# Performance work log

Hardware: AMD Instinct MI355X
Metric: run time of the kernel (lower is better)

Reference implementation:

```python
import jax, jax.numpy as jnp
import numpy as np


def gcn_conv(x, src, dst, W, b, n_nodes):
    """PyG GCNConv: out = D^-1/2 (A+I) D^-1/2 (x @ W) + b.
    src/dst already include self loops. Shapes: x [N,F], src/dst [E+N].
    """
    h = x @ W  # [N, H] - linear transform first (PyG order)
    # symmetric normalization from (unweighted) degree of A + I
    deg = jax.ops.segment_sum(jnp.ones_like(dst, dtype=h.dtype), dst,
                              num_segments=n_nodes)  # [N]
    dis = jnp.where(deg > 0, jax.lax.rsqrt(deg), 0.0)  # deg_inv_sqrt, inf->0
    norm = dis[src] * dis[dst]  # [E+N]
    msg = h[src] * norm[:, None]  # gather + scale  [E+N, H]
    out = jax.ops.segment_sum(msg, dst, num_segments=n_nodes)  # scatter-add
    return out + b


def setup_inputs() -> dict:
    key = jax.random.key(0)
    ks = jax.random.split(key, 4)
    N, E, F, H, C = 50000, 1600000, 768, 128, 2
    x = jax.random.normal(ks[0], (N, F), dtype=jnp.float32)
    edge_index = jax.random.randint(ks[1], (2, E), 0, N, dtype=jnp.int64)
    W1 = jax.random.normal(ks[2], (F, H), dtype=jnp.float32) * (1.0 / np.sqrt(F))
    b1 = jnp.zeros((H,), dtype=jnp.float32)
    W2 = jax.random.normal(ks[3], (H, C), dtype=jnp.float32) * (1.0 / np.sqrt(H))
    b2 = jnp.zeros((C,), dtype=jnp.float32)
    return {"x": x, "edge_index": edge_index, "W1": W1, "b1": b1,
            "W2": W2, "b2": b2}


def reference(x, edge_index, W1, b1, W2, b2):
    n_nodes = x.shape[0]
    # add self loops once (PyG GCNConv default add_self_loops=True)
    loops = jnp.arange(n_nodes, dtype=edge_index.dtype)
    src = jnp.concatenate([edge_index[0], loops])
    dst = jnp.concatenate([edge_index[1], loops])
    h = jax.nn.relu(gcn_conv(x, src, dst, W1, b1, n_nodes))
    h = gcn_conv(h, src, dst, W2, b2, n_nodes)
    return jax.nn.softmax(h, axis=-1)
```

## Files before the change

### kernel.cpp

```cpp
#include <hip/hip_runtime.h>
#include <hip/hip_bf16.h>
#include <stdint.h>

#define F_IN 768
#define H_DIM 128
#define CAP 128

typedef __attribute__((ext_vector_type(8))) short short8;
typedef __attribute__((ext_vector_type(4))) float floatx4;

__device__ __forceinline__ unsigned short f2bf(float f) {
    union { float f; unsigned u; } v; v.f = f;
    unsigned r = v.u + 0x7fff + ((v.u >> 16) & 1);
    return (unsigned short)(r >> 16);
}
__device__ __forceinline__ float bflo(unsigned u) {
    union { unsigned u; float f; } v; v.u = u << 16;
    return v.f;
}
__device__ __forceinline__ float bfhi(unsigned u) {
    union { unsigned u; float f; } v; v.u = u & 0xffff0000u;
    return v.f;
}

__global__ void k_init(int* __restrict__ cnt, int N,
                       const float* __restrict__ W1, unsigned short* __restrict__ W1B) {
    int t = blockIdx.x * blockDim.x + threadIdx.x;
    if (t < N) cnt[t] = 0;
    if (t < 8 * 24 * 64) {
        int lane = t & 63;
        int kb = (t >> 6) % 24;
        int f  = (t >> 6) / 24;
        int r = lane & 15, quad = lane >> 4;
        int col = f * 16 + r;
        int k0 = kb * 32 + quad * 8;
        unsigned short* o = W1B + (size_t)t * 8;
#pragma unroll
        for (int j = 0; j < 8; j++) o[j] = f2bf(W1[(size_t)(k0 + j) * H_DIM + col]);
    }
}

__global__ __launch_bounds__(256) void k_build(const int* __restrict__ ei, int E, int N,
                                               int* __restrict__ cnt, int* __restrict__ csr) {
    int g = blockIdx.x & 7;
    int r = blockIdx.x >> 3;
    int nbg = gridDim.x >> 3;
    int span = (N + 7) >> 3;
    int lo = g * span, hi = min(lo + span, N);
    for (int e = r * 256 + threadIdx.x; e < E; e += nbg * 256) {
        int d = ei[E + e];
        d = min(max(d, 0), N - 1);
        if (d >= lo && d < hi) {
            int s = ei[e];
            s = min(max(s, 0), N - 1);
            int pos = atomicAdd(&cnt[d], 1);
            if (pos < CAP) csr[(size_t)d * CAP + pos] = s;
        }
    }
}

__global__ void k_dis(const int* __restrict__ cnt, float* __restrict__ dis, int N) {
    int i = blockIdx.x * blockDim.x + threadIdx.x;
    if (i < N) dis[i] = rsqrtf((float)(cnt[i] + 1));
}

#define CH6 128
#define S6 140

#define LOAD6(vv, c)                                                     \
    { _Pragma("unroll")                                                  \
      for (int j = 0; j < 4; j++)                                        \
          vv[j] = *(const floatx4*)(rp[j] + (c) * CH6); }

#define STORE6(b, vv)                                                    \
    { _Pragma("unroll")                                                  \
      for (int j = 0; j < 4; j++) {                                      \
          uint2 w;                                                       \
          w.x = (unsigned)f2bf(vv[j][0]) | ((unsigned)f2bf(vv[j][1]) << 16); \
          w.y = (unsigned)f2bf(vv[j][2]) | ((unsigned)f2bf(vv[j][3]) << 16); \
          *(uint2*)(&As[b][woff[j]]) = w; } }

#define MFMA6(b, c)                                                      \
    { _Pragma("unroll")                                                  \
      for (int kk = 0; kk < 4; kk++) {                                   \
          short8 af0 = *(const short8*)(&As[b][r * S6 + kk * 32 + quad * 8]);        \
          short8 af1 = *(const short8*)(&As[b][(16 + r) * S6 + kk * 32 + quad * 8]); \
          int kbg = (c) * 4 + kk;                                        \
          short8 b0 = *(const short8*)(bp + kbg * 512);                  \
          short8 b1 = *(const short8*)(bp + 12288 + kbg * 512);          \
          acc00 = __builtin_amdgcn_mfma_f32_16x16x32_bf16(af0, b0, acc00, 0, 0, 0); \
          acc01 = __builtin_amdgcn_mfma_f32_16x16x32_bf16(af0, b1, acc01, 0, 0, 0); \
          acc10 = __builtin_amdgcn_mfma_f32_16x16x32_bf16(af1, b0, acc10, 0, 0, 0); \
          acc11 = __builtin_amdgcn_mfma_f32_16x16x32_bf16(af1, b1, acc11, 0, 0, 0); } }

__global__ __launch_bounds__(256, 3) void k_gemm1(const float* __restrict__ x,
                                                  const unsigned short* __restrict__ W1B,
                                                  unsigned short* __restrict__ h, int N) {
    __shared__ unsigned short As[2][32 * S6];
    int rowblk = blockIdx.x * 32;
    int tid = threadIdx.x;
    int wv = tid >> 6;
    int lane = tid & 63;
    int quad = lane >> 4;
    int r = lane & 15;

    const float* rp[4];
    int woff[4];
#pragma unroll
    for (int j = 0; j < 4; j++) {
        int idx = j * 256 + tid;
        int row = idx >> 5, c4 = idx & 31;
        int sr = min(rowblk + row, N - 1);
        rp[j] = x + (size_t)sr * F_IN + c4 * 4;
        woff[j] = row * S6 + c4 * 4;
    }

    const unsigned short* bp = W1B + ((size_t)(2 * wv) * 24 * 512) + (size_t)lane * 8;

    floatx4 acc00 = (floatx4){0.f, 0.f, 0.f, 0.f};
    floatx4 acc01 = (floatx4){0.f, 0.f, 0.f, 0.f};
    floatx4 acc10 = (floatx4){0.f, 0.f, 0.f, 0.f};
    floatx4 acc11 = (floatx4){0.f, 0.f, 0.f, 0.f};

    floatx4 v0[4], v1[4], v2[4];

    LOAD6(v0, 0); LOAD6(v1, 1); LOAD6(v2, 2);
    STORE6(0, v0);
    __syncthreads();

    LOAD6(v0, 3); MFMA6(0, 0); STORE6(1, v1); __syncthreads();
    LOAD6(v1, 4); MFMA6(1, 1); STORE6(0, v2); __syncthreads();
    LOAD6(v2, 5); MFMA6(0, 2); STORE6(1, v0); __syncthreads();
    MFMA6(1, 3); STORE6(0, v1); __syncthreads();
    MFMA6(0, 4); STORE6(1, v2); __syncthreads();
    MFMA6(1, 5);

    int c0 = (2 * wv) * 16 + r, c1 = (2 * wv + 1) * 16 + r;
#pragma unroll
    for (int i = 0; i < 4; i++) {
        int orow0 = rowblk + quad * 4 + i;
        int orow1 = orow0 + 16;
        if (orow0 < N) {
            h[(size_t)orow0 * H_DIM + c0] = f2bf(acc00[i]);
            h[(size_t)orow0 * H_DIM + c1] = f2bf(acc01[i]);
        }
        if (orow1 < N) {
            h[(size_t)orow1 * H_DIM + c0] = f2bf(acc10[i]);
            h[(size_t)orow1 * H_DIM + c1] = f2bf(acc11[i]);
        }
    }
}

__global__ __launch_bounds__(256) void k_agg1(const unsigned short* __restrict__ h,
                                              const int* __restrict__ csr,
                                              const int* __restrict__ cnt,
                                              const float* __restrict__ dis,
                                              const float* __restrict__ b1,
                                              const float* __restrict__ W2,
                                              float* __restrict__ h2, int N) {
    int wv = (blockIdx.x * blockDim.x + threadIdx.x) >> 6;
    if (wv >= N) return;
    int lane = threadIdx.x & 63;
    int c = lane & 15;
    int p = lane >> 4;
    int nedge = min(cnt[wv], CAP);
    int beg = wv * CAP;
    float dv = dis[wv];

    uint4 hs = *(const uint4*)(h + (size_t)wv * H_DIM + 8 * c);
    float sf = (p == 0) ? dv : 0.f;
    float a0 = sf * bflo(hs.x), a1 = sf * bfhi(hs.x);
    float a2 = sf * bflo(hs.y), a3 = sf * bfhi(hs.y);
    float a4 = sf * bflo(hs.z), a5 = sf * bfhi(hs.z);
    float a6 = sf * bflo(hs.w), a7 = sf * bfhi(hs.w);

    for (int j0 = 0; j0 < nedge; j0 += 64) {
        int idx = j0 + lane;
        bool valid = idx < nedge;
        int u = csr[valid ? (beg + idx) : beg];
        float du = valid ? dis[u] : 0.f;
        int cnt64 = nedge - j0; if (cnt64 > 64) cnt64 = 64;
        int quads = (cnt64 + 3) >> 2;
        for (int t = 0; t < quads; t++) {
            int srcl = 4 * t + p;
            int uu = __shfl(u, srcl);
            float dd = __shfl(du, srcl);
            uint4 hv = *(const uint4*)(h + (size_t)uu * H_DIM + 8 * c);
            a0 += dd * bflo(hv.x); a1 += dd * bfhi(hv.x);
            a2 += dd * bflo(hv.y); a3 += dd * bfhi(hv.y);
            a4 += dd * bflo(hv.z); a5 += dd * bfhi(hv.z);
            a6 += dd * bflo(hv.w); a7 += dd * bfhi(hv.w);
        }
    }
    a0 += __shfl_xor(a0, 16); a0 += __shfl_xor(a0, 32);
    a1 += __shfl_xor(a1, 16); a1 += __shfl_xor(a1, 32);
    a2 += __shfl_xor(a2, 16); a2 += __shfl_xor(a2, 32);
    a3 += __shfl_xor(a3, 16); a3 += __shfl_xor(a3, 32);
    a4 += __shfl_xor(a4, 16); a4 += __shfl_xor(a4, 32);
    a5 += __shfl_xor(a5, 16); a5 += __shfl_xor(a5, 32);
    a6 += __shfl_xor(a6, 16); a6 += __shfl_xor(a6, 32);
    a7 += __shfl_xor(a7, 16); a7 += __shfl_xor(a7, 32);

    floatx4 bb0 = *(const floatx4*)(b1 + 8 * c);
    floatx4 bb1 = *(const floatx4*)(b1 + 8 * c + 4);
    float h0 = fmaxf(a0 * dv + bb0[0], 0.f);
    float h1 = fmaxf(a1 * dv + bb0[1], 0.f);
    float h2a = fmaxf(a2 * dv + bb0[2], 0.f);
    float h3 = fmaxf(a3 * dv + bb0[3], 0.f);
    float h4 = fmaxf(a4 * dv + bb1[0], 0.f);
    float h5 = fmaxf(a5 * dv + bb1[1], 0.f);
    float h6 = fmaxf(a6 * dv + bb1[2], 0.f);
    float h7 = fmaxf(a7 * dv + bb1[3], 0.f);
    const float* w2p = W2 + 16 * c;
    floatx4 wA = *(const floatx4*)(w2p);
    floatx4 wB = *(const floatx4*)(w2p + 4);
    floatx4 wC = *(const floatx4*)(w2p + 8);
    floatx4 wD = *(const floatx4*)(w2p + 12);
    float p0 = h0 * wA[0] + h1 * wA[2] + h2a * wB[0] + h3 * wB[2]
             + h4 * wC[0] + h5 * wC[2] + h6 * wD[0] + h7 * wD[2];
    float p1 = h0 * wA[1] + h1 * wA[3] + h2a * wB[1] + h3 * wB[3]
             + h4 * wC[1] + h5 * wC[3] + h6 * wD[1] + h7 * wD[3];
#pragma unroll
    for (int m = 8; m >= 1; m >>= 1) {
        p0 += __shfl_xor(p0, m);
        p1 += __shfl_xor(p1, m);
    }
    if (lane == 0) {
        h2[(size_t)wv * 2]     = p0;
        h2[(size_t)wv * 2 + 1] = p1;
    }
}

__global__ __launch_bounds__(256) void k_agg2sm(const int* __restrict__ csr,
                                                const int* __restrict__ cnt,
                                                const float* __restrict__ dis,
                                                const float* __restrict__ h2,
                                                const float* __restrict__ b2,
                                                float* __restrict__ out, int N) {
    int i = (blockIdx.x * blockDim.x + threadIdx.x) >> 4;
    if (i >= N) return;
    int l = threadIdx.x & 15;
    int nedge = min(cnt[i], CAP);
    int beg = i * CAP;
    float dv = dis[i];
    float2 hself = *(const float2*)(h2 + (size_t)i * 2);
    float sf = (l == 0) ? dv : 0.f;
    float a0 = sf * hself.x, a1 = sf * hself.y;
    for (int j = l; j < nedge; j += 16) {
        int u = csr[beg + j];
        float w = dis[u];
        float2 hv = *(const float2*)(h2 + (size_t)u * 2);
        a0 += w * hv.x;
        a1 += w * hv.y;
    }
#pragma unroll
    for (int m = 8; m >= 1; m >>= 1) {
        a0 += __shfl_xor(a0, m);
        a1 += __shfl_xor(a1, m);
    }
    if (l == 0) {
        float o0 = a0 * dv + b2[0];
        float o1 = a1 * dv + b2[1];
        float m = fmaxf(o0, o1);
        float e0 = __expf(o0 - m), e1 = __expf(o1 - m);
        float inv = 1.f / (e0 + e1);
        float2 r; r.x = e0 * inv; r.y = e1 * inv;
        *(float2*)(out + (size_t)i * 2) = r;
    }
}

extern "C" void kernel_launch(void* const* d_in, const int* in_sizes, int n_in,
                              void* d_out, int out_size, void* d_ws, size_t ws_size,
                              hipStream_t stream) {
    const float* x  = (const float*)d_in[0];
    const int*   ei = (const int*)d_in[1];
    const float* W1 = (const float*)d_in[2];
    const float* b1 = (const float*)d_in[3];
    const float* W2 = (const float*)d_in[4];
    const float* b2 = (const float*)d_in[5];
    int N = in_sizes[0] / F_IN;
    int E = in_sizes[1] / 2;

    char* p = (char*)d_ws;
    auto alloc = [&](size_t bytes) {
        void* q = (void*)p;
        p += (bytes + 255) & ~(size_t)255;
        return q;
    };
    int* cnt              = (int*)alloc((size_t)N * 4);
    int* csr              = (int*)alloc((size_t)N * CAP * 4);
    float* dis            = (float*)alloc((size_t)N * 4);
    unsigned short* W1B   = (unsigned short*)alloc((size_t)F_IN * H_DIM * 2);
    unsigned short* h     = (unsigned short*)alloc((size_t)N * H_DIM * 2);
    float* h2             = (float*)alloc((size_t)N * 2 * 4);
    float* out            = (float*)d_out;

    k_init<<<(N + 255) / 256, 256, 0, stream>>>(cnt, N, W1, W1B);
    k_build<<<2048, 256, 0, stream>>>(ei, E, N, cnt, csr);
    k_dis<<<(N + 255) / 256, 256, 0, stream>>>(cnt, dis, N);
    k_gemm1<<<(N + 31) / 32, 256, 0, stream>>>(x, W1B, h, N);
    k_agg1<<<(N + 3) / 4, 256, 0, stream>>>(h, csr, cnt, dis, b1, W2, h2, N);
    k_agg2sm<<<(N * 16 + 255) / 256, 256, 0, stream>>>(csr, cnt, dis, h2, b2, out, N);
}
```

Before: 393.2 us.

## Enlarge GEMM1 row tile to 64 rows with double-buffered register prefetch

```diff
diff --git a/kernel.cpp b/kernel.cpp
--- a/kernel.cpp
+++ b/kernel.cpp
@@ -69,12 +69,13 @@
 
 #define LOAD6(vv, c)                                                     \
     { _Pragma("unroll")                                                  \
-      for (int j = 0; j < 4; j++)                                        \
-          vv[j] = *(const floatx4*)(rp[j] + (c) * CH6); }
+      for (int j = 0; j < 8; j++)                                        \
+          vv[j] = *(const floatx4*)(rp[j] + (c) * CH6);                  \
+      __builtin_amdgcn_sched_barrier(0); }
 
 #define STORE6(b, vv)                                                    \
     { _Pragma("unroll")                                                  \
-      for (int j = 0; j < 4; j++) {                                      \
+      for (int j = 0; j < 8; j++) {                                      \
           uint2 w;                                                       \
           w.x = (unsigned)f2bf(vv[j][0]) | ((unsigned)f2bf(vv[j][1]) << 16); \
           w.y = (unsigned)f2bf(vv[j][2]) | ((unsigned)f2bf(vv[j][3]) << 16); \
@@ -83,31 +84,31 @@
 #define MFMA6(b, c)                                                      \
     { _Pragma("unroll")                                                  \
       for (int kk = 0; kk < 4; kk++) {                                   \
-          short8 af0 = *(const short8*)(&As[b][r * S6 + kk * 32 + quad * 8]);        \
-          short8 af1 = *(const short8*)(&As[b][(16 + r) * S6 + kk * 32 + quad * 8]); \
           int kbg = (c) * 4 + kk;                                        \
           short8 b0 = *(const short8*)(bp + kbg * 512);                  \
           short8 b1 = *(const short8*)(bp + 12288 + kbg * 512);          \
-          acc00 = __builtin_amdgcn_mfma_f32_16x16x32_bf16(af0, b0, acc00, 0, 0, 0); \
-          acc01 = __builtin_amdgcn_mfma_f32_16x16x32_bf16(af0, b1, acc01, 0, 0, 0); \
-          acc10 = __builtin_amdgcn_mfma_f32_16x16x32_bf16(af1, b0, acc10, 0, 0, 0); \
-          acc11 = __builtin_amdgcn_mfma_f32_16x16x32_bf16(af1, b1, acc11, 0, 0, 0); } }
+          _Pragma("unroll")                                              \
+          for (int rt = 0; rt < 4; rt++) {                               \
+              short8 af = *(const short8*)(&As[b][(rt * 16 + r) * S6 + kk * 32 + quad * 8]); \
+              acc[rt][0] = __builtin_amdgcn_mfma_f32_16x16x32_bf16(af, b0, acc[rt][0], 0, 0, 0); \
+              acc[rt][1] = __builtin_amdgcn_mfma_f32_16x16x32_bf16(af, b1, acc[rt][1], 0, 0, 0); \
+          } } }
 
 __global__ __launch_bounds__(256, 3) void k_gemm1(const float* __restrict__ x,
                                                   const unsigned short* __restrict__ W1B,
                                                   unsigned short* __restrict__ h, int N) {
-    __shared__ unsigned short As[2][32 * S6];
-    int rowblk = blockIdx.x * 32;
+    __shared__ unsigned short As[2][64 * S6];
+    int rowblk = blockIdx.x * 64;
     int tid = threadIdx.x;
     int wv = tid >> 6;
     int lane = tid & 63;
     int quad = lane >> 4;
     int r = lane & 15;
 
-    const float* rp[4];
-    int woff[4];
-#pragma unroll
-    for (int j = 0; j < 4; j++) {
+    const float* rp[8];
+    int woff[8];
+#pragma unroll
+    for (int j = 0; j < 8; j++) {
         int idx = j * 256 + tid;
         int row = idx >> 5, c4 = idx & 31;
         int sr = min(rowblk + row, N - 1);
@@ -117,36 +118,36 @@
 
     const unsigned short* bp = W1B + ((size_t)(2 * wv) * 24 * 512) + (size_t)lane * 8;
 
-    floatx4 acc00 = (floatx4){0.f, 0.f, 0.f, 0.f};
-    floatx4 acc01 = (floatx4){0.f, 0.f, 0.f, 0.f};
-    floatx4 acc10 = (floatx4){0.f, 0.f, 0.f, 0.f};
-    floatx4 acc11 = (floatx4){0.f, 0.f, 0.f, 0.f};
-
-    floatx4 v0[4], v1[4], v2[4];
-
-    LOAD6(v0, 0); LOAD6(v1, 1); LOAD6(v2, 2);
+    floatx4 acc[4][2];
+#pragma unroll
+    for (int rt = 0; rt < 4; rt++) {
+        acc[rt][0] = (floatx4){0.f, 0.f, 0.f, 0.f};
+        acc[rt][1] = (floatx4){0.f, 0.f, 0.f, 0.f};
+    }
+
+    floatx4 v0[8], v1[8];
+
+    LOAD6(v0, 0); LOAD6(v1, 1);
     STORE6(0, v0);
     __syncthreads();
 
-    LOAD6(v0, 3); MFMA6(0, 0); STORE6(1, v1); __syncthreads();
-    LOAD6(v1, 4); MFMA6(1, 1); STORE6(0, v2); __syncthreads();
-    LOAD6(v2, 5); MFMA6(0, 2); STORE6(1, v0); __syncthreads();
-    MFMA6(1, 3); STORE6(0, v1); __syncthreads();
-    MFMA6(0, 4); STORE6(1, v2); __syncthreads();
+    LOAD6(v0, 2); MFMA6(0, 0); STORE6(1, v1); __syncthreads();
+    LOAD6(v1, 3); MFMA6(1, 1); STORE6(0, v0); __syncthreads();
+    LOAD6(v0, 4); MFMA6(0, 2); STORE6(1, v1); __syncthreads();
+    LOAD6(v1, 5); MFMA6(1, 3); STORE6(0, v0); __syncthreads();
+    MFMA6(0, 4); STORE6(1, v1); __syncthreads();
     MFMA6(1, 5);
 
     int c0 = (2 * wv) * 16 + r, c1 = (2 * wv + 1) * 16 + r;
 #pragma unroll
-    for (int i = 0; i < 4; i++) {
-        int orow0 = rowblk + quad * 4 + i;
-        int orow1 = orow0 + 16;
-        if (orow0 < N) {
-            h[(size_t)orow0 * H_DIM + c0] = f2bf(acc00[i]);
-            h[(size_t)orow0 * H_DIM + c1] = f2bf(acc01[i]);
-        }
-        if (orow1 < N) {
-            h[(size_t)orow1 * H_DIM + c0] = f2bf(acc10[i]);
-            h[(size_t)orow1 * H_DIM + c1] = f2bf(acc11[i]);
+    for (int rt = 0; rt < 4; rt++) {
+#pragma unroll
+        for (int i = 0; i < 4; i++) {
+            int orow = rowblk + rt * 16 + quad * 4 + i;
+            if (orow < N) {
+                h[(size_t)orow * H_DIM + c0] = f2bf(acc[rt][0][i]);
+                h[(size_t)orow * H_DIM + c1] = f2bf(acc[rt][1][i]);
+            }
         }
     }
 }
@@ -298,7 +299,7 @@
     k_init<<<(N + 255) / 256, 256, 0, stream>>>(cnt, N, W1, W1B);
     k_build<<<2048, 256, 0, stream>>>(ei, E, N, cnt, csr);
     k_dis<<<(N + 255) / 256, 256, 0, stream>>>(cnt, dis, N);
-    k_gemm1<<<(N + 31) / 32, 256, 0, stream>>>(x, W1B, h, N);
+    k_gemm1<<<(N + 63) / 64, 256, 0, stream>>>(x, W1B, h, N);
     k_agg1<<<(N + 3) / 4, 256, 0, stream>>>(h, csr, cnt, dis, b1, W2, h2, N);
     k_agg2sm<<<(N * 16 + 255) / 256, 256, 0, stream>>>(csr, cnt, dis, h2, b2, out, N);
 }
```

After: 398.6 us. About the same (+1.4%).
